# Kernel optimization log

Hardware: AMD Instinct MI355X
Metric: run time of the kernel (lower is better)

Reference implementation:

```python
import jax, jax.numpy as jnp
import numpy as np

N = 80000   # active voxels
G = 64      # voxel grid side
K = 27      # 3x3x3 kernel taps


def _build_coord_maps():
    """Random unique voxel coords in a G^3 grid; 27-tap neighbor index map (-1 = missing)."""
    rng = np.random.default_rng(0)
    flat = rng.choice(G ** 3, size=N, replace=False).astype(np.int64)
    coords = np.stack(np.unravel_index(flat, (G, G, G)), axis=1)  # (N,3)
    order = np.argsort(flat)
    skeys = flat[order]
    offs = [(dx, dy, dz) for dx in (-1, 0, 1) for dy in (-1, 0, 1) for dz in (-1, 0, 1)]
    nbr = np.full((K, N), -1, np.int32)
    for k, (dx, dy, dz) in enumerate(offs):
        nc = coords + np.array([dx, dy, dz])
        inb = np.all((nc >= 0) & (nc < G), axis=1)
        nkey = nc[:, 0] * G * G + nc[:, 1] * G + nc[:, 2]
        pos = np.clip(np.searchsorted(skeys, nkey), 0, N - 1)
        hit = inb & (skeys[pos] == nkey)
        nbr[k] = np.where(hit, order[pos], -1)
    return nbr


_W_SPECS = [('a1w', (27, 96, 64)), ('a2w', (64, 64)), ('a3w', (27, 64, 64)), ('a4w', (64, 64)),
            ('b1w', (27, 256, 64)), ('b2w', (64, 64)), ('b3w', (27, 64, 32)), ('b4w', (32, 32)),
            ('c1w', (27, 96, 128)), ('c2w', (128, 128)), ('c3w', (128, 128))]
_BN_SPECS = [('a1', 64), ('a2', 64), ('a3', 64), ('a4', 64),
             ('b1', 64), ('b2', 64), ('b3', 32), ('b4', 32),
             ('c1', 128), ('c2', 128), ('c3', 128)]


def setup_inputs() -> dict:
    key = jax.random.key(0)
    ks = jax.random.split(key, 64)
    inp = {
        'feat3d': jax.random.normal(ks[0], (N, 96), jnp.float32),
        'feat2d': jax.random.normal(ks[1], (N, 256), jnp.float32),
    }
    i = 2
    for name, shp in _W_SPECS:
        fan = float(np.prod(shp[:-1]))
        inp[name] = jax.random.normal(ks[i], shp, jnp.float32) * (1.0 / np.sqrt(fan))
        i += 1
    for pre, c in _BN_SPECS:  # folded eval-mode BN: y = x*scale + shift
        inp[pre + 's'] = 1.0 + 0.1 * jax.random.normal(ks[i], (c,), jnp.float32)
        inp[pre + 'b'] = 0.1 * jax.random.normal(ks[i + 1], (c,), jnp.float32)
        i += 2
    inp['nbr_idx'] = jnp.asarray(_build_coord_maps())
    inp['align_idx'] = jnp.arange(N, dtype=jnp.int32)  # 2D/3D share coordinates -> exact match
    return inp


def _sconv(x, W, nbr):
    """Sparse 3x3x3 conv: per-tap masked gather + GEMM, accumulated (gather-GEMM-scatter)."""
    out = jnp.zeros((x.shape[0], W.shape[-1]), x.dtype)
    for k in range(W.shape[0]):
        idx = nbr[k]
        g = jnp.where((idx >= 0)[:, None], x[jnp.maximum(idx, 0)], 0.0)
        out = out + g @ W[k]
    return out


def _bnrelu(x, s, b):
    return jax.nn.relu(x * s + b)


def reference(feat3d, feat2d,
              a1w, a2w, a3w, a4w, b1w, b2w, b3w, b4w, c1w, c2w, c3w,
              a1s, a1b, a2s, a2b, a3s, a3b, a4s, a4b,
              b1s, b1b, b2s, b2b, b3s, b3b, b4s, b4b,
              c1s, c1b, c2s, c2b, c3s, c3b,
              nbr_idx, align_idx):
    # 3D branch: 96 -> 64 (dropout = identity in eval)
    x = _bnrelu(_sconv(feat3d, a1w, nbr_idx), a1s, a1b)
    x = _bnrelu(x @ a2w, a2s, a2b)
    x = _bnrelu(_sconv(x, a3w, nbr_idx), a3s, a3b)
    x3 = _bnrelu(x @ a4w, a4s, a4b)
    # 2D branch: 256 -> 32
    y = _bnrelu(_sconv(feat2d, b1w, nbr_idx), b1s, b1b)
    y = _bnrelu(y @ b2w, b2s, b2b)
    y = _bnrelu(_sconv(y, b3w, nbr_idx), b3s, b3b)
    y2 = _bnrelu(y @ b4w, b4s, b4b)
    # features_at_coordinates: exact-match gather at the 3D coords, NaN/Inf -> 0
    ya = y2[align_idx]
    ya = jnp.where(jnp.isfinite(ya), ya, 0.0)
    # fusion: concat 64+32=96 -> 128
    z = jnp.concatenate([x3, ya], axis=1)
    z = _bnrelu(_sconv(z, c1w, nbr_idx), c1s, c1b)
    z = _bnrelu(z @ c2w, c2s, c2b)
    z = _bnrelu(z @ c3w, c3s, c3b)
    return z
```

## Files before the change

kernel.cpp:

```cpp
#include <hip/hip_runtime.h>

typedef __bf16 bf16;
typedef __bf16 bf16x8 __attribute__((ext_vector_type(8)));
typedef __bf16 bf16x4 __attribute__((ext_vector_type(4)));
typedef float  f32x4  __attribute__((ext_vector_type(4)));

__global__ void f2b_kernel(const float* __restrict__ src, bf16* __restrict__ dst, int n4) {
    int i = blockIdx.x * 256 + threadIdx.x;
    if (i >= n4) return;
    float4 v = ((const float4*)src)[i];
    bf16x4 o = { (bf16)v.x, (bf16)v.y, (bf16)v.z, (bf16)v.w };
    ((bf16x4*)dst)[i] = o;
}

__global__ void swz_kernel(const float* __restrict__ W, bf16* __restrict__ Wf,
                           int cin, int cout, int total) {
    int e = blockIdx.x * 256 + threadIdx.x;
    if (e >= total) return;
    int per_tap = cin * cout;
    int tap = e / per_tap;
    int t2  = e - tap * per_tap;
    int ntc = cout >> 4;
    int s   = t2 / (ntc * 512);
    int r3  = t2 - s * (ntc * 512);
    int nt  = r3 >> 9;
    int L   = (r3 & 511) >> 3;
    int j   = r3 & 7;
    int k   = s * 32 + (L >> 4) * 8 + j;
    int col = nt * 16 + (L & 15);
    Wf[e] = (bf16)W[((size_t)tap * cin + k) * cout + col];
}

template<int CIN, int C1, int TAPS, int C2, int C3>
__global__ __launch_bounds__(256, 3) void layer_kernel(
    const bf16* __restrict__ X,
    const bf16* __restrict__ W1,
    const bf16* __restrict__ W2,
    const bf16* __restrict__ W3,
    const int*  __restrict__ nbr,
    const float* __restrict__ sc1, const float* __restrict__ sh1,
    const float* __restrict__ sc2, const float* __restrict__ sh2,
    const float* __restrict__ sc3, const float* __restrict__ sh3,
    bf16* __restrict__ Y, float* __restrict__ Yf,
    int ystride, int yoff, int n, int nblocks)
{
    constexpr int NT1 = C1 / 16;
    constexpr int WC1 = NT1;
    constexpr int RW  = (C1 >= 128) ? 32 : 64;
    constexpr int WR1 = RW / 16;
    constexpr int KS  = CIN / 32;
    constexpr int LS1 = C1 + 8;
    constexpr int LS2 = C2 + 8;
    constexpr int HC  = C1 / 2;
    constexpr int HCP = HC + 1;
    constexpr int PRB = 4 * RW * HCP * 4;
    constexpr int LTB = RW * LS1 * 2;
    constexpr bool BPRE = (WC1 <= 4);

    __shared__ __align__(16) char smem[PRB + LTB];
    float* PR  = (float*)smem;
    bf16*  Lt  = (bf16*)(smem + PRB);
    bf16*  Lt2 = (bf16*)smem;

    const int tid  = threadIdx.x;
    const int lane = tid & 63;
    const int wv   = tid >> 6;
    const int m16  = lane & 15;
    const int quad = lane >> 4;

    const int bq = nblocks >> 3, br = nblocks & 7;
    const int bx = blockIdx.x & 7, bs = blockIdx.x >> 3;
    const int sb = bx * bq + (bx < br ? bx : br) + bs;
    const int base = sb * RW;

    constexpr int TB = TAPS / 4, TR = TAPS % 4;
    const int tstart = wv * TB + (wv < TR ? wv : TR);
    const int tcnt   = TB + (wv < TR ? 1 : 0);
    const int TOTW   = tcnt * KS;

    const bf16x8 ZB = __builtin_bit_cast(bf16x8, (float4){0.f, 0.f, 0.f, 0.f});

    int idxc[WR1], idxn[WR1];
    auto load_idx = [&](int t, int (&id)[WR1]) {
#pragma unroll
        for (int r = 0; r < WR1; ++r)
            id[r] = nbr[(size_t)t * n + base + r * 16 + m16];
    };
    auto load_b = [&](int gstep, bf16x8 (&b)[WC1]) {
        const bf16* wt = W1 + (size_t)gstep * (NT1 * 512) + lane * 8;
#pragma unroll
        for (int c = 0; c < WC1; ++c)
            b[c] = *(const bf16x8*)(wt + c * 512);
    };

    f32x4 acc1[WR1][WC1];
#pragma unroll
    for (int r = 0; r < WR1; ++r)
#pragma unroll
        for (int c = 0; c < WC1; ++c) acc1[r][c] = (f32x4){0.f, 0.f, 0.f, 0.f};

    bf16x8 aA[WR1], aB[WR1], bA[WC1], bB[WC1];

    load_idx(tstart, idxc);
    if (tcnt > 1) load_idx(tstart + 1, idxn);
    if constexpr (BPRE) load_b(tstart * KS, bA);
#pragma unroll
    for (int r = 0; r < WR1; ++r) {
        bf16x8 v = ZB;
        if (idxc[r] >= 0) v = *(const bf16x8*)(X + (size_t)(unsigned)idxc[r] * CIN + quad * 8);
        aA[r] = v;
    }

    int tloc = 0, s = 0;
    auto dostep = [&](int it, bf16x8 (&aC)[WR1], bf16x8 (&bC)[WC1],
                      bf16x8 (&aN)[WR1], bf16x8 (&bN)[WC1]) {
        int s1 = s + 1, tl1 = tloc;
        bool wrap = (s1 == KS);
        if (wrap) { s1 = 0; ++tl1; }
        if (it + 1 < TOTW) {
            if constexpr (BPRE) load_b((tstart + tl1) * KS + s1, bN);
#pragma unroll
            for (int r = 0; r < WR1; ++r) {
                int id_ = wrap ? idxn[r] : idxc[r];
                bf16x8 v = ZB;
                if (id_ >= 0) v = *(const bf16x8*)(X + (size_t)(unsigned)id_ * CIN + s1 * 32 + quad * 8);
                aN[r] = v;
            }
        }
        if constexpr (!BPRE) load_b((tstart + tloc) * KS + s, bC);
#pragma unroll
        for (int r = 0; r < WR1; ++r)
#pragma unroll
            for (int c = 0; c < WC1; ++c)
                acc1[r][c] = __builtin_amdgcn_mfma_f32_16x16x32_bf16(aC[r], bC[c], acc1[r][c], 0, 0, 0);
        if (wrap) {
#pragma unroll
            for (int r = 0; r < WR1; ++r) idxc[r] = idxn[r];
            if (tloc + 2 < tcnt) load_idx(tstart + tloc + 2, idxn);
        }
        tloc = tl1; s = s1;
    };

    for (int it = 0; it < TOTW; it += 2) {
        dostep(it, aA, bA, aB, bB);
        if (it + 1 < TOTW) dostep(it + 1, aB, bB, aA, bA);
    }

    constexpr int SLICE = RW / 4;
#pragma unroll
    for (int p = 0; p < 2; ++p) {
        __syncthreads();
        float* Pw = PR + wv * (RW * HCP);
#pragma unroll
        for (int c = 0; c < WC1 / 2; ++c)
#pragma unroll
            for (int r = 0; r < WR1; ++r)
#pragma unroll
                for (int i = 0; i < 4; ++i)
                    Pw[(r * 16 + quad * 4 + i) * HCP + c * 16 + m16] = acc1[r][p * (WC1 / 2) + c][i];
        __syncthreads();
#pragma unroll
        for (int e = lane; e < SLICE * HC; e += 64) {
            int row  = wv * SLICE + e / HC;
            int colh = e & (HC - 1);
            float v = PR[(0 * RW + row) * HCP + colh] + PR[(1 * RW + row) * HCP + colh]
                    + PR[(2 * RW + row) * HCP + colh] + PR[(3 * RW + row) * HCP + colh];
            int col = p * HC + colh;
            v = v * sc1[col] + sh1[col];
            v = v > 0.f ? v : 0.f;
            Lt[row * LS1 + col] = (bf16)v;
        }
    }
    __syncthreads();

    constexpr int NT2  = C2 / 16;
    constexpr int DRW  = RW / 16 >= 4 ? 4 : RW / 16;
    constexpr int NCG  = 4 / DRW;
    constexpr int WC2g = NT2 / NCG;
    constexpr int KS2  = C1 / 32;
    const int wr  = wv % DRW;
    const int wcg = wv / DRW;

    f32x4 acc2[WC2g];
#pragma unroll
    for (int c = 0; c < WC2g; ++c) acc2[c] = (f32x4){0.f, 0.f, 0.f, 0.f};

#pragma unroll
    for (int s2 = 0; s2 < KS2; ++s2) {
        bf16x8 a = *(const bf16x8*)(&Lt[(wr * 16 + m16) * LS1 + s2 * 32 + quad * 8]);
        bf16x8 bw[WC2g];
#pragma unroll
        for (int c = 0; c < WC2g; ++c)
            bw[c] = *(const bf16x8*)(W2 + ((s2 * NT2 + wcg * WC2g + c) * 512 + lane * 8));
#pragma unroll
        for (int c = 0; c < WC2g; ++c)
            acc2[c] = __builtin_amdgcn_mfma_f32_16x16x32_bf16(a, bw[c], acc2[c], 0, 0, 0);
    }

    if constexpr (C3 == 0) {
#pragma unroll
        for (int c = 0; c < WC2g; ++c) {
            int col = (wcg * WC2g + c) * 16 + m16;
            float sc = sc2[col], sh = sh2[col];
            int row0 = base + wr * 16 + quad * 4;
#pragma unroll
            for (int i = 0; i < 4; ++i) {
                float v = acc2[c][i] * sc + sh;
                v = v > 0.f ? v : 0.f;
                size_t off = (size_t)(row0 + i) * ystride + yoff + col;
                if (Yf) Yf[off] = v;
                else    Y[off] = (bf16)v;
            }
        }
    } else {
#pragma unroll
        for (int c = 0; c < WC2g; ++c) {
            int col = (wcg * WC2g + c) * 16 + m16;
            float sc = sc2[col], sh = sh2[col];
            int row0 = wr * 16 + quad * 4;
#pragma unroll
            for (int i = 0; i < 4; ++i) {
                float v = acc2[c][i] * sc + sh;
                v = v > 0.f ? v : 0.f;
                Lt2[(row0 + i) * LS2 + col] = (bf16)v;
            }
        }
        __syncthreads();

        constexpr int C3v  = (C3 > 0) ? C3 : 16;
        constexpr int NT3  = C3v / 16;
        constexpr int WC3g = NT3 / NCG;
        constexpr int KS3  = C2 / 32;

        f32x4 acc3[WC3g];
#pragma unroll
        for (int c = 0; c < WC3g; ++c) acc3[c] = (f32x4){0.f, 0.f, 0.f, 0.f};

#pragma unroll
        for (int s3 = 0; s3 < KS3; ++s3) {
            bf16x8 a = *(const bf16x8*)(&Lt2[(wr * 16 + m16) * LS2 + s3 * 32 + quad * 8]);
            bf16x8 bw[WC3g];
#pragma unroll
            for (int c = 0; c < WC3g; ++c)
                bw[c] = *(const bf16x8*)(W3 + ((s3 * NT3 + wcg * WC3g + c) * 512 + lane * 8));
#pragma unroll
            for (int c = 0; c < WC3g; ++c)
                acc3[c] = __builtin_amdgcn_mfma_f32_16x16x32_bf16(a, bw[c], acc3[c], 0, 0, 0);
        }

#pragma unroll
        for (int c = 0; c < WC3g; ++c) {
            int col = (wcg * WC3g + c) * 16 + m16;
            float sc = sc3[col], sh = sh3[col];
            int row0 = base + wr * 16 + quad * 4;
#pragma unroll
            for (int i = 0; i < 4; ++i) {
                float v = acc3[c][i] * sc + sh;
                v = v > 0.f ? v : 0.f;
                size_t off = (size_t)(row0 + i) * ystride + yoff + col;
                if (Yf) Yf[off] = v;
                else    Y[off] = (bf16)v;
            }
        }
    }
}

__global__ void concat_kernel(const bf16* __restrict__ y2, const int* __restrict__ align,
                              bf16* __restrict__ z, int n) {
    int e = blockIdx.x * 256 + threadIdx.x;
    if (e >= n * 32) return;
    int i = e >> 5, c = e & 31;
    int a = align[i];
    float v = (float)y2[(size_t)a * 32 + c];
    unsigned u = __builtin_bit_cast(unsigned, v);
    if ((u & 0x7f800000u) == 0x7f800000u) v = 0.f;
    z[(size_t)i * 96 + 64 + c] = (bf16)v;
}

extern "C" void kernel_launch(void* const* d_in, const int* in_sizes, int n_in,
                              void* d_out, int out_size, void* d_ws, size_t ws_size,
                              hipStream_t stream) {
    const float* feat3d = (const float*)d_in[0];
    const float* feat2d = (const float*)d_in[1];
    const float* Wsrc[11];
    for (int i = 0; i < 11; ++i) Wsrc[i] = (const float*)d_in[2 + i];
    const float* bn[22];
    for (int i = 0; i < 22; ++i) bn[i] = (const float*)d_in[13 + i];
    const int* nbr   = (const int*)d_in[35];
    const int* align = (const int*)d_in[36];
    float* out = (float*)d_out;

    const int n = in_sizes[0] / 96;

    char* ws = (char*)d_ws;
    size_t off = 0;
    auto alloc = [&](size_t bytes) -> void* {
        void* p = ws + off;
        off = (off + bytes + 255) & ~(size_t)255;
        return p;
    };
    bf16* F3 = (bf16*)alloc((size_t)n * 96 * 2);
    bf16* F2 = (bf16*)alloc((size_t)n * 256 * 2);
    static const int wt_taps[11] = {27, 1, 27, 1, 27, 1, 27, 1, 27, 1, 1};
    static const int wt_cin[11]  = {96, 64, 64, 64, 256, 64, 64, 32, 96, 128, 128};
    static const int wt_cout[11] = {64, 64, 64, 64, 64, 64, 32, 32, 128, 128, 128};
    bf16* Wf[11];
    for (int i = 0; i < 11; ++i)
        Wf[i] = (bf16*)alloc((size_t)wt_taps[i] * wt_cin[i] * wt_cout[i] * 2);
    bf16* tA = (bf16*)alloc((size_t)n * 64 * 2);
    bf16* tB = (bf16*)alloc((size_t)n * 64 * 2);
    bf16* y2 = (bf16*)alloc((size_t)n * 32 * 2);
    bf16* z  = (bf16*)alloc((size_t)n * 96 * 2);

    f2b_kernel<<<(n * 96 / 4 + 255) / 256, 256, 0, stream>>>(feat3d, F3, n * 96 / 4);
    f2b_kernel<<<(n * 256 / 4 + 255) / 256, 256, 0, stream>>>(feat2d, F2, n * 256 / 4);
    for (int i = 0; i < 11; ++i) {
        int total = wt_taps[i] * wt_cin[i] * wt_cout[i];
        swz_kernel<<<(total + 255) / 256, 256, 0, stream>>>(Wsrc[i], Wf[i], wt_cin[i], wt_cout[i], total);
    }

    const int GB64 = n / 64;
    const int GB32 = n / 32;

    layer_kernel<96, 64, 27, 64, 0><<<GB64, 256, 0, stream>>>(
        F3, Wf[0], Wf[1], nullptr, nbr,
        bn[0], bn[1], bn[2], bn[3], nullptr, nullptr,
        tB, nullptr, 64, 0, n, GB64);
    layer_kernel<64, 64, 27, 64, 0><<<GB64, 256, 0, stream>>>(
        tB, Wf[2], Wf[3], nullptr, nbr,
        bn[4], bn[5], bn[6], bn[7], nullptr, nullptr,
        z, nullptr, 96, 0, n, GB64);

    layer_kernel<256, 64, 27, 64, 0><<<GB64, 256, 0, stream>>>(
        F2, Wf[4], Wf[5], nullptr, nbr,
        bn[8], bn[9], bn[10], bn[11], nullptr, nullptr,
        tA, nullptr, 64, 0, n, GB64);
    layer_kernel<64, 32, 27, 32, 0><<<GB64, 256, 0, stream>>>(
        tA, Wf[6], Wf[7], nullptr, nbr,
        bn[12], bn[13], bn[14], bn[15], nullptr, nullptr,
        y2, nullptr, 32, 0, n, GB64);

    concat_kernel<<<(n * 32 + 255) / 256, 256, 0, stream>>>(y2, align, z, n);

    layer_kernel<96, 128, 27, 128, 128><<<GB32, 256, 0, stream>>>(
        z, Wf[8], Wf[9], Wf[10], nbr,
        bn[16], bn[17], bn[18], bn[19], bn[20], bn[21],
        nullptr, out, 128, 0, n, GB32);
}
```

Before: 589.9 us.

## Stream weight fragments per MFMA pair and shrink reduction staging for occupancy

Drops the double-buffered weight register arrays. B fragments are now loaded two at a time right before their MFMAs, with s_setprio raised around the MMA block. The cross-wave partial-sum reduction runs in 2 or 4 passes depending on width, which shrinks LDS staging. Launch bounds go from 3 to 4 blocks per CU. Together this cuts register and LDS pressure to raise occupancy, at the cost of exposing weight-load latency directly before each MFMA group.

```diff
diff --git a/kernel.cpp b/kernel.cpp
--- a/kernel.cpp
+++ b/kernel.cpp
@@ -32,7 +32,7 @@
 }
 
 template<int CIN, int C1, int TAPS, int C2, int C3>
-__global__ __launch_bounds__(256, 3) void layer_kernel(
+__global__ __launch_bounds__(256, 4) void layer_kernel(
     const bf16* __restrict__ X,
     const bf16* __restrict__ W1,
     const bf16* __restrict__ W2,
@@ -51,11 +51,12 @@
     constexpr int KS  = CIN / 32;
     constexpr int LS1 = C1 + 8;
     constexpr int LS2 = C2 + 8;
-    constexpr int HC  = C1 / 2;
-    constexpr int HCP = HC + 1;
-    constexpr int PRB = 4 * RW * HCP * 4;
+    constexpr int NP  = (WC1 >= 4) ? 4 : 2;
+    constexpr int CPF = WC1 / NP;
+    constexpr int CP  = 16 * CPF;
+    constexpr int CPS = CP + 1;
+    constexpr int PRB = 4 * RW * CPS * 4;
     constexpr int LTB = RW * LS1 * 2;
-    constexpr bool BPRE = (WC1 <= 4);
 
     __shared__ __align__(16) char smem[PRB + LTB];
     float* PR  = (float*)smem;
@@ -86,12 +87,6 @@
         for (int r = 0; r < WR1; ++r)
             id[r] = nbr[(size_t)t * n + base + r * 16 + m16];
     };
-    auto load_b = [&](int gstep, bf16x8 (&b)[WC1]) {
-        const bf16* wt = W1 + (size_t)gstep * (NT1 * 512) + lane * 8;
-#pragma unroll
-        for (int c = 0; c < WC1; ++c)
-            b[c] = *(const bf16x8*)(wt + c * 512);
-    };
 
     f32x4 acc1[WR1][WC1];
 #pragma unroll
@@ -99,11 +94,10 @@
 #pragma unroll
         for (int c = 0; c < WC1; ++c) acc1[r][c] = (f32x4){0.f, 0.f, 0.f, 0.f};
 
-    bf16x8 aA[WR1], aB[WR1], bA[WC1], bB[WC1];
+    bf16x8 aA[WR1], aB[WR1];
 
     load_idx(tstart, idxc);
     if (tcnt > 1) load_idx(tstart + 1, idxn);
-    if constexpr (BPRE) load_b(tstart * KS, bA);
 #pragma unroll
     for (int r = 0; r < WR1; ++r) {
         bf16x8 v = ZB;
@@ -112,13 +106,11 @@
     }
 
     int tloc = 0, s = 0;
-    auto dostep = [&](int it, bf16x8 (&aC)[WR1], bf16x8 (&bC)[WC1],
-                      bf16x8 (&aN)[WR1], bf16x8 (&bN)[WC1]) {
+    auto dostep = [&](int it, bf16x8 (&aC)[WR1], bf16x8 (&aN)[WR1]) {
         int s1 = s + 1, tl1 = tloc;
         bool wrap = (s1 == KS);
         if (wrap) { s1 = 0; ++tl1; }
         if (it + 1 < TOTW) {
-            if constexpr (BPRE) load_b((tstart + tl1) * KS + s1, bN);
 #pragma unroll
             for (int r = 0; r < WR1; ++r) {
                 int id_ = wrap ? idxn[r] : idxc[r];
@@ -127,12 +119,20 @@
                 aN[r] = v;
             }
         }
-        if constexpr (!BPRE) load_b((tstart + tloc) * KS + s, bC);
-#pragma unroll
-        for (int r = 0; r < WR1; ++r)
-#pragma unroll
-            for (int c = 0; c < WC1; ++c)
-                acc1[r][c] = __builtin_amdgcn_mfma_f32_16x16x32_bf16(aC[r], bC[c], acc1[r][c], 0, 0, 0);
+        const bf16* wt = W1 + (size_t)((tstart + tloc) * KS + s) * (NT1 * 512) + lane * 8;
+        __builtin_amdgcn_s_setprio(1);
+#pragma unroll
+        for (int cg = 0; cg < WC1; cg += 2) {
+            bf16x8 b0 = *(const bf16x8*)(wt + cg * 512);
+            bf16x8 b1 = *(const bf16x8*)(wt + (cg + 1) * 512);
+#pragma unroll
+            for (int r = 0; r < WR1; ++r)
+                acc1[r][cg]     = __builtin_amdgcn_mfma_f32_16x16x32_bf16(aC[r], b0, acc1[r][cg], 0, 0, 0);
+#pragma unroll
+            for (int r = 0; r < WR1; ++r)
+                acc1[r][cg + 1] = __builtin_amdgcn_mfma_f32_16x16x32_bf16(aC[r], b1, acc1[r][cg + 1], 0, 0, 0);
+        }
+        __builtin_amdgcn_s_setprio(0);
         if (wrap) {
 #pragma unroll
             for (int r = 0; r < WR1; ++r) idxc[r] = idxn[r];
@@ -142,30 +142,30 @@
     };
 
     for (int it = 0; it < TOTW; it += 2) {
-        dostep(it, aA, bA, aB, bB);
-        if (it + 1 < TOTW) dostep(it + 1, aB, bB, aA, bA);
+        dostep(it, aA, aB);
+        if (it + 1 < TOTW) dostep(it + 1, aB, aA);
     }
 
     constexpr int SLICE = RW / 4;
 #pragma unroll
-    for (int p = 0; p < 2; ++p) {
+    for (int p = 0; p < NP; ++p) {
         __syncthreads();
-        float* Pw = PR + wv * (RW * HCP);
-#pragma unroll
-        for (int c = 0; c < WC1 / 2; ++c)
+        float* Pw = PR + wv * (RW * CPS);
+#pragma unroll
+        for (int c = 0; c < CPF; ++c)
 #pragma unroll
             for (int r = 0; r < WR1; ++r)
 #pragma unroll
                 for (int i = 0; i < 4; ++i)
-                    Pw[(r * 16 + quad * 4 + i) * HCP + c * 16 + m16] = acc1[r][p * (WC1 / 2) + c][i];
+                    Pw[(r * 16 + quad * 4 + i) * CPS + c * 16 + m16] = acc1[r][p * CPF + c][i];
         __syncthreads();
 #pragma unroll
-        for (int e = lane; e < SLICE * HC; e += 64) {
-            int row  = wv * SLICE + e / HC;
-            int colh = e & (HC - 1);
-            float v = PR[(0 * RW + row) * HCP + colh] + PR[(1 * RW + row) * HCP + colh]
-                    + PR[(2 * RW + row) * HCP + colh] + PR[(3 * RW + row) * HCP + colh];
-            int col = p * HC + colh;
+        for (int e = lane; e < SLICE * CP; e += 64) {
+            int row  = wv * SLICE + e / CP;
+            int colh = e & (CP - 1);
+            float v = PR[(0 * RW + row) * CPS + colh] + PR[(1 * RW + row) * CPS + colh]
+                    + PR[(2 * RW + row) * CPS + colh] + PR[(3 * RW + row) * CPS + colh];
+            int col = p * CP + colh;
             v = v * sc1[col] + sh1[col];
             v = v > 0.f ? v : 0.f;
             Lt[row * LS1 + col] = (bf16)v;
```

Result: slower. 722.6 us (+22.5%).

## Split first-stage conv waves across column groups and taps for wide outputs

Applied to the files above, without the earlier changes.

For wide first-stage outputs (more than four 16-column tiles), the four waves are now split into two column groups times two tap groups instead of four tap groups that each cover all columns. This halves per-wave accumulator registers and B-fragment loads, and always prefetches weight fragments. The cross-wave reduction is reorganised to sum over fewer tap partials per column slice with a smaller LDS scratch. MFMA sections are wrapped in s_setprio so compute waves get issue priority. The trade-off is that activation gathers are duplicated across the column-group waves.

```diff
diff --git a/kernel.cpp b/kernel.cpp
--- a/kernel.cpp
+++ b/kernel.cpp
@@ -44,22 +44,26 @@
     bf16* __restrict__ Y, float* __restrict__ Yf,
     int ystride, int yoff, int n, int nblocks)
 {
-    constexpr int NT1 = C1 / 16;
-    constexpr int WC1 = NT1;
-    constexpr int RW  = (C1 >= 128) ? 32 : 64;
-    constexpr int WR1 = RW / 16;
-    constexpr int KS  = CIN / 32;
-    constexpr int LS1 = C1 + 8;
-    constexpr int LS2 = C2 + 8;
-    constexpr int HC  = C1 / 2;
-    constexpr int HCP = HC + 1;
-    constexpr int PRB = 4 * RW * HCP * 4;
-    constexpr int LTB = RW * LS1 * 2;
-    constexpr bool BPRE = (WC1 <= 4);
-
-    __shared__ __align__(16) char smem[PRB + LTB];
+    constexpr int NT1  = C1 / 16;
+    constexpr int NCG1 = (NT1 > 4) ? 2 : 1;
+    constexpr int WC1  = NT1 / NCG1;
+    constexpr int TW   = 4 / NCG1;
+    constexpr int RW   = (C1 >= 128) ? 32 : 64;
+    constexpr int WR1  = RW / 16;
+    constexpr int KS   = CIN / 32;
+    constexpr int LS1  = C1 + 8;
+    constexpr int LS2  = C2 + 8;
+    constexpr int NP   = WC1;
+    constexpr int CPT  = 16 * NCG1;
+    constexpr int PCW  = CPT + 1;
+    constexpr int PRB  = TW * RW * PCW * 4;
+    constexpr int L2TB = (C3 > 0) ? RW * LS2 * 2 : 0;
+    constexpr int REG  = (PRB > L2TB) ? PRB : L2TB;
+    constexpr int LTB  = RW * LS1 * 2;
+
+    __shared__ __align__(16) char smem[REG + LTB];
     float* PR  = (float*)smem;
-    bf16*  Lt  = (bf16*)(smem + PRB);
+    bf16*  Lt  = (bf16*)(smem + REG);
     bf16*  Lt2 = (bf16*)smem;
 
     const int tid  = threadIdx.x;
@@ -67,15 +71,17 @@
     const int wv   = tid >> 6;
     const int m16  = lane & 15;
     const int quad = lane >> 4;
+    const int tg   = wv % TW;
+    const int cg   = wv / TW;
 
     const int bq = nblocks >> 3, br = nblocks & 7;
     const int bx = blockIdx.x & 7, bs = blockIdx.x >> 3;
     const int sb = bx * bq + (bx < br ? bx : br) + bs;
     const int base = sb * RW;
 
-    constexpr int TB = TAPS / 4, TR = TAPS % 4;
-    const int tstart = wv * TB + (wv < TR ? wv : TR);
-    const int tcnt   = TB + (wv < TR ? 1 : 0);
+    constexpr int TB = TAPS / TW, TR = TAPS % TW;
+    const int tstart = tg * TB + (tg < TR ? tg : TR);
+    const int tcnt   = TB + (tg < TR ? 1 : 0);
     const int TOTW   = tcnt * KS;
 
     const bf16x8 ZB = __builtin_bit_cast(bf16x8, (float4){0.f, 0.f, 0.f, 0.f});
@@ -87,7 +93,7 @@
             id[r] = nbr[(size_t)t * n + base + r * 16 + m16];
     };
     auto load_b = [&](int gstep, bf16x8 (&b)[WC1]) {
-        const bf16* wt = W1 + (size_t)gstep * (NT1 * 512) + lane * 8;
+        const bf16* wt = W1 + (size_t)gstep * (NT1 * 512) + (cg * WC1) * 512 + lane * 8;
 #pragma unroll
         for (int c = 0; c < WC1; ++c)
             b[c] = *(const bf16x8*)(wt + c * 512);
@@ -103,7 +109,7 @@
 
     load_idx(tstart, idxc);
     if (tcnt > 1) load_idx(tstart + 1, idxn);
-    if constexpr (BPRE) load_b(tstart * KS, bA);
+    load_b(tstart * KS, bA);
 #pragma unroll
     for (int r = 0; r < WR1; ++r) {
         bf16x8 v = ZB;
@@ -118,7 +124,7 @@
         bool wrap = (s1 == KS);
         if (wrap) { s1 = 0; ++tl1; }
         if (it + 1 < TOTW) {
-            if constexpr (BPRE) load_b((tstart + tl1) * KS + s1, bN);
+            load_b((tstart + tl1) * KS + s1, bN);
 #pragma unroll
             for (int r = 0; r < WR1; ++r) {
                 int id_ = wrap ? idxn[r] : idxc[r];
@@ -127,12 +133,13 @@
                 aN[r] = v;
             }
         }
-        if constexpr (!BPRE) load_b((tstart + tloc) * KS + s, bC);
+        __builtin_amdgcn_s_setprio(1);
 #pragma unroll
         for (int r = 0; r < WR1; ++r)
 #pragma unroll
             for (int c = 0; c < WC1; ++c)
                 acc1[r][c] = __builtin_amdgcn_mfma_f32_16x16x32_bf16(aC[r], bC[c], acc1[r][c], 0, 0, 0);
+        __builtin_amdgcn_s_setprio(0);
         if (wrap) {
 #pragma unroll
             for (int r = 0; r < WR1; ++r) idxc[r] = idxn[r];
@@ -148,24 +155,24 @@
 
     constexpr int SLICE = RW / 4;
 #pragma unroll
-    for (int p = 0; p < 2; ++p) {
+    for (int p = 0; p < NP; ++p) {
         __syncthreads();
-        float* Pw = PR + wv * (RW * HCP);
-#pragma unroll
-        for (int c = 0; c < WC1 / 2; ++c)
-#pragma unroll
-            for (int r = 0; r < WR1; ++r)
-#pragma unroll
-                for (int i = 0; i < 4; ++i)
-                    Pw[(r * 16 + quad * 4 + i) * HCP + c * 16 + m16] = acc1[r][p * (WC1 / 2) + c][i];
+        float* Pw = PR + tg * (RW * PCW);
+#pragma unroll
+        for (int r = 0; r < WR1; ++r)
+#pragma unroll
+            for (int i = 0; i < 4; ++i)
+                Pw[(r * 16 + quad * 4 + i) * PCW + cg * 16 + m16] = acc1[r][p][i];
         __syncthreads();
 #pragma unroll
-        for (int e = lane; e < SLICE * HC; e += 64) {
-            int row  = wv * SLICE + e / HC;
-            int colh = e & (HC - 1);
-            float v = PR[(0 * RW + row) * HCP + colh] + PR[(1 * RW + row) * HCP + colh]
-                    + PR[(2 * RW + row) * HCP + colh] + PR[(3 * RW + row) * HCP + colh];
-            int col = p * HC + colh;
+        for (int e = lane; e < SLICE * CPT; e += 64) {
+            int row   = wv * SLICE + e / CPT;
+            int colsl = e & (CPT - 1);
+            float v = 0.f;
+#pragma unroll
+            for (int g = 0; g < TW; ++g)
+                v += PR[(g * RW + row) * PCW + colsl];
+            int col = ((colsl >> 4) * WC1 + p) * 16 + (colsl & 15);
             v = v * sc1[col] + sh1[col];
             v = v > 0.f ? v : 0.f;
             Lt[row * LS1 + col] = (bf16)v;
```

After: 585.5 us. Within noise of the previous version (-0.7%).
